# Performance work log

Measured on AMD Instinct MI355X. Metric: run time of the kernel, lower is better.

The kernel has to match this reference:

```python
import jax, jax.numpy as jnp
import numpy as np
from jax import lax

BN_EPS = 1e-5


def ste_sign(t):
    # sign() binarization with straight-through estimator (identity grad),
    # matching BinarizeConv2d which binarizes .data in-place.
    return t + lax.stop_gradient(jnp.sign(t) - t)


def setup_inputs() -> dict:
    key = jax.random.key(0)
    k1, k2, k3, k4 = jax.random.split(key, 4)
    N, C, H, W = 128, 256, 28, 28
    x = jax.random.normal(k1, (N, C, H, W), dtype=jnp.float32)
    w = jax.random.normal(k2, (C, C, 3, 3), dtype=jnp.float32)  # OIHW
    gamma = jnp.ones((C,), dtype=jnp.float32)
    beta = jnp.zeros((C,), dtype=jnp.float32)
    running_mean = jax.random.normal(k3, (C,), dtype=jnp.float32)
    running_var = jax.random.uniform(k4, (C,), dtype=jnp.float32)
    return {"x": x, "w": w, "gamma": gamma, "beta": beta,
            "running_mean": running_mean, "running_var": running_var}


def reference(x, w, gamma, beta, running_mean, running_var):
    residual = x
    # Binarize activations and weights to {-1, 0, +1} via sign (0 measure-zero for randn)
    xb = ste_sign(x)
    wb = ste_sign(w)
    # 3x3 conv, stride 1, padding 1, no bias
    out = lax.conv_general_dilated(
        xb, wb, window_strides=(1, 1), padding=((1, 1), (1, 1)),
        dimension_numbers=("NCHW", "OIHW", "NCHW"))
    # BatchNorm2d (inference form with running stats), per-channel affine
    inv = gamma / jnp.sqrt(running_var + BN_EPS)  # [C]
    out = out * inv[None, :, None, None] + (beta - running_mean * inv)[None, :, None, None]
    # Hardtanh
    out = jnp.clip(out, -1.0, 1.0)
    # residual add (downsample is None)
    return out + residual
```

## Files before the change

kernel.cpp:

```cpp
#include <hip/hip_runtime.h>
#include <stdint.h>

typedef unsigned long long u64;

#define N_ 128
#define C_ 256
#define H_ 28
#define W_ 28
#define BN_EPS_ 1e-5f

__global__ __launch_bounds__(256) void pack_x_kernel(const float* __restrict__ x,
                                                     u64* __restrict__ xbits) {
    int gid  = blockIdx.x * blockDim.x + threadIdx.x;
    int wave = gid >> 6;
    int lane = gid & 63;
    int k    = wave & 3;
    int nh   = wave >> 2;
    if (nh >= N_ * H_) return;
    int h = nh % H_;
    int n = nh / H_;
    int c = k * 64 + lane;
    const float* xp = x + (((size_t)n * C_ + c) * H_ + h) * W_;

    u64 my = 0;
    #pragma unroll
    for (int w = 0; w < W_; ++w) {
        u64 mask = __ballot(xp[w] < 0.f);
        if (lane == w) my = mask;
    }
    if (lane < W_) xbits[((size_t)nh * W_ + lane) * 4 + k] = my;
}

__global__ __launch_bounds__(256) void pack_w_kernel(const float* __restrict__ w,
                                                     u64* __restrict__ wbits) {
    int gid  = blockIdx.x * blockDim.x + threadIdx.x;
    int wave = gid >> 6;
    int lane = gid & 63;
    if (wave >= C_ * 9 * 4) return;
    int k    = wave & 3;
    int rest = wave >> 2;
    int tap  = rest % 9;
    int co   = rest / 9;
    int ci   = k * 64 + lane;
    float val = w[((size_t)co * C_ + ci) * 9 + tap];
    u64 mask = __ballot(val < 0.f);
    if (lane == 0) wbits[wave] = mask;
}

__global__ __launch_bounds__(256) void conv_kernel(
    const u64* __restrict__ xbits, const u64* __restrict__ wbits,
    const float* __restrict__ x,
    const float* __restrict__ gamma, const float* __restrict__ beta,
    const float* __restrict__ mean, const float* __restrict__ var,
    float* __restrict__ out) {
    int nh = blockIdx.x;
    int h  = nh % H_;
    int n  = nh / H_;
    int co = threadIdx.x;

    __shared__ union {
        u64   lx[3][W_][4];
        float sout[C_][29];
    } sm;

    float inv  = gamma[co] / sqrtf(var[co] + BN_EPS_);
    float bias = beta[co] - mean[co] * inv;

    u64 wr[9][4];
    {
        const ulonglong2* wp = (const ulonglong2*)wbits + (size_t)co * 18;
        #pragma unroll
        for (int i = 0; i < 9; ++i) {
            ulonglong2 a = wp[i * 2];
            ulonglong2 b = wp[i * 2 + 1];
            wr[i][0] = a.x; wr[i][1] = a.y; wr[i][2] = b.x; wr[i][3] = b.y;
        }
    }

    for (int i = threadIdx.x; i < 3 * W_ * 4; i += 256) {
        int k    = i & 3;
        int rest = i >> 2;
        int ww   = rest % W_;
        int r    = rest / W_;
        int ih   = h - 1 + r;
        u64 v = 0;
        if (ih >= 0 && ih < H_)
            v = xbits[(((size_t)n * H_ + ih) * W_ + ww) * 4 + k];
        sm.lx[r][ww][k] = v;
    }
    __syncthreads();

    const bool row0 = (h > 0);
    const bool row2 = (h < H_ - 1);
    const int  nrows = 1 + (row0 ? 1 : 0) + (row2 ? 1 : 0);

    int sacc[W_];
    int pm = 0, pc = 0;

    for (int iw = 0; iw < W_; ++iw) {
        int a0 = 0, a1 = 0, a2 = 0;
        u64 xw0, xw1, xw2, xw3;
        #define TAPROW(r, wb)                                                  \
            xw0 = sm.lx[r][iw][0]; xw1 = sm.lx[r][iw][1];                      \
            xw2 = sm.lx[r][iw][2]; xw3 = sm.lx[r][iw][3];                      \
            a0 += __popcll(xw0 ^ wr[wb+0][0]) + __popcll(xw1 ^ wr[wb+0][1]) +  \
                  __popcll(xw2 ^ wr[wb+0][2]) + __popcll(xw3 ^ wr[wb+0][3]);   \
            a1 += __popcll(xw0 ^ wr[wb+1][0]) + __popcll(xw1 ^ wr[wb+1][1]) +  \
                  __popcll(xw2 ^ wr[wb+1][2]) + __popcll(xw3 ^ wr[wb+1][3]);   \
            a2 += __popcll(xw0 ^ wr[wb+2][0]) + __popcll(xw1 ^ wr[wb+2][1]) +  \
                  __popcll(xw2 ^ wr[wb+2][2]) + __popcll(xw3 ^ wr[wb+2][3]);
        if (row0) { TAPROW(0, 0) }
        { TAPROW(1, 3) }
        if (row2) { TAPROW(2, 6) }
        #undef TAPROW
        if (iw >= 1) sacc[iw - 1] = pm + a2;
        pm = pc + a1;
        pc = a0;
    }
    sacc[W_ - 1] = pm;

    __syncthreads();

    #pragma unroll
    for (int w = 0; w < W_; ++w) {
        int ncols = 3 - (w == 0 ? 1 : 0) - (w == W_ - 1 ? 1 : 0);
        int nv    = C_ * nrows * ncols;
        float convv = (float)(nv - 2 * sacc[w]);
        float val   = convv * inv + bias;
        val = fminf(1.f, fmaxf(-1.f, val));
        sm.sout[co][w] = val;
    }
    __syncthreads();

    const float* xplane = x   + ((size_t)n * C_ * H_ + h) * W_;
    float*       oplane = out + ((size_t)n * C_ * H_ + h) * W_;
    for (int i = threadIdx.x; i < C_ * W_; i += 256) {
        int c    = i / W_;
        int wpos = i - c * W_;
        size_t g = (size_t)c * (H_ * W_) + wpos;
        oplane[g] = sm.sout[c][wpos] + xplane[g];
    }
}

extern "C" void kernel_launch(void* const* d_in, const int* in_sizes, int n_in,
                              void* d_out, int out_size, void* d_ws, size_t ws_size,
                              hipStream_t stream) {
    const float* x     = (const float*)d_in[0];
    const float* w     = (const float*)d_in[1];
    const float* gamma = (const float*)d_in[2];
    const float* beta  = (const float*)d_in[3];
    const float* mean  = (const float*)d_in[4];
    const float* var   = (const float*)d_in[5];
    float* out = (float*)d_out;

    u64* xbits = (u64*)d_ws;
    u64* wbits = xbits + (size_t)N_ * H_ * W_ * 4;

    int pack_x_threads = N_ * H_ * 4 * 64;
    pack_x_kernel<<<(pack_x_threads + 255) / 256, 256, 0, stream>>>(x, xbits);
    pack_w_kernel<<<(C_ * 9 * 4 * 64) / 256, 256, 0, stream>>>(w, wbits);
    conv_kernel<<<N_ * H_, 256, 0, stream>>>(xbits, wbits, x, gamma, beta, mean, var, out);
}
```

Before: 325.7 us.

## Repack x bits per-thread with float2 loads and fully unroll conv loop

The activation packing kernel changes from per-row wave ballots to each thread reading 64 channels for two adjacent pixels with float2 loads and building two bitmasks with shifts, which coalesces reads across pixels. The conv kernel gains a launch_bounds occupancy hint of 3 blocks and a fully unrolled width loop so the sacc array can stay in registers. The trade-off is more serial work per thread in packing, and register pressure or spills from the unroll under the tighter occupancy limit.

After: 335.6 us. 1.03x slower.

```diff
diff --git a/kernel.cpp b/kernel.cpp
--- a/kernel.cpp
+++ b/kernel.cpp
@@ -7,28 +7,29 @@
 #define C_ 256
 #define H_ 28
 #define W_ 28
+#define NPIX_ (N_ * H_ * W_)
 #define BN_EPS_ 1e-5f
 
 __global__ __launch_bounds__(256) void pack_x_kernel(const float* __restrict__ x,
                                                      u64* __restrict__ xbits) {
-    int gid  = blockIdx.x * blockDim.x + threadIdx.x;
-    int wave = gid >> 6;
-    int lane = gid & 63;
-    int k    = wave & 3;
-    int nh   = wave >> 2;
-    if (nh >= N_ * H_) return;
-    int h = nh % H_;
-    int n = nh / H_;
-    int c = k * 64 + lane;
-    const float* xp = x + (((size_t)n * C_ + c) * H_ + h) * W_;
+    int tid = blockIdx.x * blockDim.x + threadIdx.x;
+    if (tid >= (NPIX_ / 2) * 4) return;
+    int k  = tid & 3;
+    int p2 = tid >> 2;
+    int g0 = p2 * 2;
+    int n  = g0 / (H_ * W_);
+    int hw = g0 - n * (H_ * W_);
+    const float* xp = x + ((size_t)n * C_ + (size_t)k * 64) * (H_ * W_) + hw;
 
-    u64 my = 0;
+    u64 b0 = 0, b1 = 0;
     #pragma unroll
-    for (int w = 0; w < W_; ++w) {
-        u64 mask = __ballot(xp[w] < 0.f);
-        if (lane == w) my = mask;
+    for (int j = 0; j < 64; ++j) {
+        float2 f = *(const float2*)(xp + (size_t)j * (H_ * W_));
+        b0 |= (u64)(f.x < 0.f) << j;
+        b1 |= (u64)(f.y < 0.f) << j;
     }
-    if (lane < W_) xbits[((size_t)nh * W_ + lane) * 4 + k] = my;
+    xbits[(size_t)g0 * 4 + k]       = b0;
+    xbits[(size_t)(g0 + 1) * 4 + k] = b1;
 }
 
 __global__ __launch_bounds__(256) void pack_w_kernel(const float* __restrict__ w,
@@ -47,7 +48,7 @@
     if (lane == 0) wbits[wave] = mask;
 }
 
-__global__ __launch_bounds__(256) void conv_kernel(
+__global__ __launch_bounds__(256, 3) void conv_kernel(
     const u64* __restrict__ xbits, const u64* __restrict__ wbits,
     const float* __restrict__ x,
     const float* __restrict__ gamma, const float* __restrict__ beta,
@@ -85,7 +86,7 @@
         int ih   = h - 1 + r;
         u64 v = 0;
         if (ih >= 0 && ih < H_)
-            v = xbits[(((size_t)n * H_ + ih) * W_ + ww) * 4 + k];
+            v = xbits[((size_t)(n * H_ + ih) * W_ + ww) * 4 + k];
         sm.lx[r][ww][k] = v;
     }
     __syncthreads();
@@ -97,6 +98,7 @@
     int sacc[W_];
     int pm = 0, pc = 0;
 
+    #pragma unroll
     for (int iw = 0; iw < W_; ++iw) {
         int a0 = 0, a1 = 0, a2 = 0;
         u64 xw0, xw1, xw2, xw3;
@@ -154,9 +156,9 @@
     float* out = (float*)d_out;
 
     u64* xbits = (u64*)d_ws;
-    u64* wbits = xbits + (size_t)N_ * H_ * W_ * 4;
+    u64* wbits = xbits + (size_t)NPIX_ * 4;
 
-    int pack_x_threads = N_ * H_ * 4 * 64;
+    int pack_x_threads = (NPIX_ / 2) * 4;
     pack_x_kernel<<<(pack_x_threads + 255) / 256, 256, 0, stream>>>(x, xbits);
     pack_w_kernel<<<(C_ * 9 * 4 * 64) / 256, 256, 0, stream>>>(w, wbits);
     conv_kernel<<<N_ * H_, 256, 0, stream>>>(xbits, wbits, x, gamma, beta, mean, var, out);
```
